# Kernel optimization log

Hardware: AMD Instinct MI355X
Metric: run time of the kernel (lower is better)

## Reference

```python
import jax, jax.numpy as jnp
import numpy as np

CE_W, BOUND_W, DICE_W, SMOOTH = 1.0, 0.1, 1.0, 1e-6


def setup_inputs() -> dict:
    key = jax.random.key(0)
    k1, k2 = jax.random.split(key)
    B, C, H, W = 8, 1, 256, 256
    logits = jax.random.normal(k1, (B, C, H, W), dtype=jnp.float32)
    target = jax.random.uniform(k2, (B, C, H, W), dtype=jnp.float32)
    return {"logits": logits, "target": target}


def _edt(fg):
    # fg: [B, H, W] bool foreground mask. Returns exact Euclidean distance
    # transform of the background (0 at foreground), matching
    # scipy.ndimage.distance_transform_edt(1 - fg).
    B, H, W = fg.shape
    INF = jnp.float32(H + W)  # larger than any in-image 1D distance

    # --- pass 1: vertical distance to nearest foreground in each column ---
    fg_t = jnp.transpose(fg, (1, 0, 2))  # [H, B, W], scan over rows

    def step(carry, fg_row):
        d = jnp.where(fg_row, 0.0, carry + 1.0)
        return d, d

    init = jnp.full((B, W), INF, dtype=jnp.float32)
    _, g_fwd = jax.lax.scan(step, init, fg_t)                 # top-down
    _, g_bwd = jax.lax.scan(step, init, fg_t, reverse=True)   # bottom-up
    g = jnp.minimum(g_fwd, g_bwd)          # [H, B, W]
    g = jnp.transpose(g, (1, 0, 2))        # [B, H, W]

    # --- pass 2: exact squared EDT per row: min_k (j-k)^2 + g[i,k]^2 ---
    j = jnp.arange(W, dtype=jnp.float32)
    offs2 = (j[:, None] - j[None, :]) ** 2                    # [W, W]
    # [B, H, Wj, Wk] intermediate -> min over k
    dt2 = jnp.min(g[:, :, None, :] ** 2 + offs2[None, None, :, :], axis=-1)
    dt = jnp.sqrt(dt2)

    # empty masks get an all-zero distance map (scipy branch in the original)
    nonempty = jnp.any(fg, axis=(1, 2))
    return jnp.where(nonempty[:, None, None], dt, 0.0)


def reference(logits, target):
    target = jnp.clip(target.astype(jnp.float32), 0.0, 1.0)

    # BCEWithLogitsLoss (mean): stable log(1 + e^x) - x*t
    ce = jnp.mean(jnp.logaddexp(0.0, logits) - logits * target)

    probs = jnp.clip(jax.nn.sigmoid(logits), SMOOTH, 1.0 - SMOOTH)

    # Dice over flattened tensors
    p, t = probs.reshape(-1), target.reshape(-1)
    inter = jnp.sum(p * t)
    dice = 1.0 - (2.0 * inter + SMOOTH) / (jnp.sum(p) + jnp.sum(t) + SMOOTH)

    # Boundary: mean(probs * EDT(target > 0.5)) -- EDT is non-differentiable data
    fg = target[:, 0] > 0.5                      # [B, H, W]
    dt = jax.lax.stop_gradient(_edt(fg))[:, None]  # [B, 1, H, W]
    boundary = jnp.mean(probs * dt)

    total = CE_W * ce + DICE_W * dice + BOUND_W * boundary
    return total, ce, dice, boundary
```

## Files before the change

kernel.cpp:

```cpp
#include <hip/hip_runtime.h>

#define BB 8
#define HH 256
#define WW 256
#define NROWS (BB * HH)
#define NTOT (BB * HH * WW)

__global__ __launch_bounds__(256) void build_masks(
    const float* __restrict__ target, unsigned* __restrict__ masks) {
  const int s = blockIdx.x;
  const int b = blockIdx.y;
  const int j = threadIdx.x;
  const float* base = target + b * (HH * WW) + s * 32 * WW + j;
  unsigned m = 0;
#pragma unroll
  for (int r = 0; r < 32; ++r)
    if (base[r * WW] > 0.5f) m |= (1u << r);
  masks[b * 2048 + s * 256 + j] = m;
}

__global__ __launch_bounds__(256) void main_kernel(
    const float* __restrict__ logits, const float* __restrict__ target,
    const unsigned* __restrict__ masks,
    float* __restrict__ partials ) {
  __shared__ float s_g2[WW];
  __shared__ float s_red[4 * 5];
  __shared__ int s_any[4];

  const int row = blockIdx.x;
  const int b = row >> 8;
  const int i = row & 255;
  const int j = threadIdx.x;
  const int rowbase = row * WW;
  const int lane = j & 63;
  const int wave = j >> 6;

  unsigned m[8];
#pragma unroll
  for (int w = 0; w < 8; ++w) m[w] = masks[b * 2048 + w * 256 + j];

  const int wi = i >> 5, r = i & 31;
  int dUp = 1 << 30, dDn = 1 << 30;
  const unsigned cur = m[wi] >> r;
  if (cur) {
    dUp = __builtin_ctz(cur);
  } else {
    int off = 32 - r;
    for (int w2 = wi + 1; w2 < 8; ++w2, off += 32)
      if (m[w2]) { dUp = off + __builtin_ctz(m[w2]); break; }
  }
  const unsigned curd = m[wi] << (31 - r);
  if (curd) {
    dDn = __builtin_clz(curd);
  } else {
    int off = r + 1;
    for (int w2 = wi - 1; w2 >= 0; --w2, off += 32)
      if (m[w2]) { dDn = off + __builtin_clz(m[w2]); break; }
  }
  const int d = min(dUp, dDn);
  s_g2[j] = (d < 256) ? (float)(d * d) : 1.0e9f;

  const unsigned many = m[0] | m[1] | m[2] | m[3] | m[4] | m[5] | m[6] | m[7];
  const int wave_any = __any(many != 0u);
  if (lane == 0) s_any[wave] = wave_any;
  __syncthreads();
  const int nonempty = s_any[0] | s_any[1] | s_any[2] | s_any[3];

  const float jf = (float)j;
  float m0 = 3.4e38f, m1 = 3.4e38f, m2 = 3.4e38f, m3 = 3.4e38f;
#pragma unroll 4
  for (int k = 0; k < WW; k += 4) {
    float d0 = jf - (float)(k + 0);
    float d1 = jf - (float)(k + 1);
    float d2 = jf - (float)(k + 2);
    float d3 = jf - (float)(k + 3);
    m0 = fminf(m0, fmaf(d0, d0, s_g2[k + 0]));
    m1 = fminf(m1, fmaf(d1, d1, s_g2[k + 1]));
    m2 = fminf(m2, fmaf(d2, d2, s_g2[k + 2]));
    m3 = fminf(m3, fmaf(d3, d3, s_g2[k + 3]));
  }
  const float mn = fminf(fminf(m0, m1), fminf(m2, m3));
  const float dt = nonempty ? sqrtf(mn) : 0.0f;

  const float x = logits[rowbase + j];
  float t = target[rowbase + j];
  t = fminf(fmaxf(t, 0.0f), 1.0f);
  const float ce = fmaxf(x, 0.0f) + log1pf(expf(-fabsf(x))) - x * t;
  float p = 1.0f / (1.0f + expf(-x));
  p = fminf(fmaxf(p, 1e-6f), 1.0f - 1e-6f);

  float v[5];
  v[0] = ce;
  v[1] = p;
  v[2] = t;
  v[3] = p * t;
  v[4] = p * dt;

#pragma unroll
  for (int q = 0; q < 5; ++q) {
    float s = v[q];
#pragma unroll
    for (int off = 32; off > 0; off >>= 1) s += __shfl_down(s, off, 64);
    if (lane == 0) s_red[wave * 5 + q] = s;
  }
  __syncthreads();
  if (j == 0) {
#pragma unroll
    for (int q = 0; q < 5; ++q) {
      const float s = s_red[q] + s_red[5 + q] + s_red[10 + q] + s_red[15 + q];
      partials[q * NROWS + row] = s;
    }
  }
}

__global__ __launch_bounds__(256) void finalize(
    const float* __restrict__ partials, float* __restrict__ out) {
  __shared__ double s_red[4 * 5];
  const int j = threadIdx.x;
  double acc[5] = {0.0, 0.0, 0.0, 0.0, 0.0};
  for (int i = j; i < NROWS; i += 256) {
#pragma unroll
    for (int q = 0; q < 5; ++q) acc[q] += (double)partials[q * NROWS + i];
  }
  const int lane = j & 63;
  const int wave = j >> 6;
#pragma unroll
  for (int q = 0; q < 5; ++q) {
    double s = acc[q];
#pragma unroll
    for (int off = 32; off > 0; off >>= 1) s += __shfl_down(s, off, 64);
    if (lane == 0) s_red[wave * 5 + q] = s;
  }
  __syncthreads();
  if (j == 0) {
    double sum[5];
#pragma unroll
    for (int q = 0; q < 5; ++q)
      sum[q] = s_red[q] + s_red[5 + q] + s_red[10 + q] + s_red[15 + q];
    const double n = (double)NTOT;
    const double ce = sum[0] / n;
    const double dice = 1.0 - (2.0 * sum[3] + 1e-6) / (sum[1] + sum[2] + 1e-6);
    const double boundary = sum[4] / n;
    const double total = 1.0 * ce + 1.0 * dice + 0.1 * boundary;
    out[0] = (float)total;
    out[1] = (float)ce;
    out[2] = (float)dice;
    out[3] = (float)boundary;
  }
}

extern "C" void kernel_launch(void* const* d_in, const int* in_sizes, int n_in,
                              void* d_out, int out_size, void* d_ws,
                              size_t ws_size, hipStream_t stream) {
  const float* logits = (const float*)d_in[0];
  const float* target = (const float*)d_in[1];
  float* out = (float*)d_out;

  char* ws = (char*)d_ws;
  unsigned* masks = (unsigned*)ws;
  float* partials = (float*)(ws + 64 * 1024);

  build_masks<<<dim3(8, 8), 256, 0, stream>>>(target, masks);
  main_kernel<<<NROWS, 256, 0, stream>>>(logits, target, masks, partials);
  finalize<<<1, 256, 0, stream>>>(partials, out);
}
```

Before: 77.13 us.

## Bound EDT row search by block-wide max vertical distance; use fast math

Computes the block-wide maximum vertical distance R with a wave shuffle reduction and a shared-memory combine. The horizontal min-search then only scans offsets in [-R, R] instead of all 256 columns, which is exact because no candidate beyond R can beat a column at distance R or less. The sigmoid and softplus now share a single fast exp, and log1p is replaced by __logf(1+e). The fast intrinsics risk small precision differences, and the new loop has a runtime trip count with a branch, so it loses the previous unrolling.

Measured after the change: 69.09 us. 1.12x faster.

```diff
diff --git a/kernel.cpp b/kernel.cpp
--- a/kernel.cpp
+++ b/kernel.cpp
@@ -26,6 +26,7 @@
   __shared__ float s_g2[WW];
   __shared__ float s_red[4 * 5];
   __shared__ int s_any[4];
+  __shared__ int s_rmax[4];
 
   const int row = blockIdx.x;
   const int b = row >> 8;
@@ -59,34 +60,33 @@
   }
   const int d = min(dUp, dDn);
   s_g2[j] = (d < 256) ? (float)(d * d) : 1.0e9f;
+  const int rj = min(d, 255);
 
   const unsigned many = m[0] | m[1] | m[2] | m[3] | m[4] | m[5] | m[6] | m[7];
   const int wave_any = __any(many != 0u);
-  if (lane == 0) s_any[wave] = wave_any;
+  int rmax = rj;
+#pragma unroll
+  for (int off = 32; off > 0; off >>= 1) rmax = max(rmax, __shfl_down(rmax, off, 64));
+  if (lane == 0) { s_any[wave] = wave_any; s_rmax[wave] = rmax; }
   __syncthreads();
   const int nonempty = s_any[0] | s_any[1] | s_any[2] | s_any[3];
+  const int R = max(max(s_rmax[0], s_rmax[1]), max(s_rmax[2], s_rmax[3]));
 
-  const float jf = (float)j;
-  float m0 = 3.4e38f, m1 = 3.4e38f, m2 = 3.4e38f, m3 = 3.4e38f;
-#pragma unroll 4
-  for (int k = 0; k < WW; k += 4) {
-    float d0 = jf - (float)(k + 0);
-    float d1 = jf - (float)(k + 1);
-    float d2 = jf - (float)(k + 2);
-    float d3 = jf - (float)(k + 3);
-    m0 = fminf(m0, fmaf(d0, d0, s_g2[k + 0]));
-    m1 = fminf(m1, fmaf(d1, d1, s_g2[k + 1]));
-    m2 = fminf(m2, fmaf(d2, d2, s_g2[k + 2]));
-    m3 = fminf(m3, fmaf(d3, d3, s_g2[k + 3]));
+  float mn = 1.0e30f;
+  for (int dlt = -R; dlt <= R; ++dlt) {
+    const int k = j + dlt;
+    if ((unsigned)k < 256u)
+      mn = fminf(mn, (float)(dlt * dlt) + s_g2[k]);
   }
-  const float mn = fminf(fminf(m0, m1), fminf(m2, m3));
   const float dt = nonempty ? sqrtf(mn) : 0.0f;
 
   const float x = logits[rowbase + j];
   float t = target[rowbase + j];
   t = fminf(fmaxf(t, 0.0f), 1.0f);
-  const float ce = fmaxf(x, 0.0f) + log1pf(expf(-fabsf(x))) - x * t;
-  float p = 1.0f / (1.0f + expf(-x));
+  const float e = __expf(-fabsf(x));
+  const float inv = 1.0f / (1.0f + e);
+  const float ce = fmaxf(x, 0.0f) + __logf(1.0f + e) - x * t;
+  float p = (x >= 0.0f) ? inv : e * inv;
   p = fminf(fmaxf(p, 1e-6f), 1.0f - 1e-6f);
 
   float v[5];
```
